# Kernel optimization log

Measured on AMD Instinct MI355X. Metric: run time of the kernel, lower is better.

Reference implementation:

```python
import jax, jax.numpy as jnp
import numpy as np

B, P, H, D, CLASSES, L = 2048, 1024, 2048, 256, 10, 10
EP = 1e-64
LOG2PI = float(np.log(2.0 * np.pi))


def setup_inputs() -> dict:
    key = jax.random.key(0)
    ks = jax.random.split(key, 16)
    s = 0.05
    return {
        "data": jax.random.normal(ks[0], (B, P), dtype=jnp.float32),
        "mask": jax.random.randint(ks[1], (B, P), 0, 2) > 0,
        "enc_w1": jax.random.normal(ks[2], (P, H), dtype=jnp.float32) * s,
        "enc_b1": jnp.zeros((H,), jnp.float32),
        "enc_w2": jax.random.normal(ks[3], (H, 2 * D), dtype=jnp.float32) * s,
        "enc_b2": jnp.zeros((2 * D,), jnp.float32),
        "dec_w1": jax.random.normal(ks[4], (D, H), dtype=jnp.float32) * s,
        "dec_b1": jnp.zeros((H,), jnp.float32),
        "dec_w2": jax.random.normal(ks[5], (H, 3 * P), dtype=jnp.float32) * s,
        "dec_b2": jnp.zeros((3 * P,), jnp.float32),
        "cls_w1": jax.random.normal(ks[6], (P, H), dtype=jnp.float32) * s,
        "cls_b1": jnp.zeros((H,), jnp.float32),
        "cls_w2": jax.random.normal(ks[7], (H, CLASSES), dtype=jnp.float32) * s,
        "cls_b2": jnp.zeros((CLASSES,), jnp.float32),
    }


def _student_t_logprob(x, loc, scale, df):
    y = (x - loc) / scale
    return (jax.lax.lgamma((df + 1.0) * 0.5) - jax.lax.lgamma(df * 0.5)
            - 0.5 * jnp.log(df * jnp.pi) - jnp.log(scale)
            - 0.5 * (df + 1.0) * jnp.log1p(y * y / df))


def reference(data, mask, enc_w1, enc_b1, enc_w2, enc_b2,
              dec_w1, dec_b1, dec_w2, dec_b2,
              cls_w1, cls_b1, cls_w2, cls_b2):
    maskf = mask.astype(data.dtype)
    key = jax.random.key(42)
    k_eps, k_t = jax.random.split(key)

    # encoder
    he = jax.nn.relu(data @ enc_w1 + enc_b1)
    out_enc = he @ enc_w2 + enc_b2                      # [B, 2D]
    mu, sig = out_enc[:, :D], jax.nn.softplus(out_enc[:, D:]) + EP

    # reparameterized q(z|x) samples, L draws
    eps = jax.random.normal(k_eps, (L, B, D), dtype=data.dtype)
    z = mu[None] + sig[None] * eps                      # [L, B, D]
    zf = z.reshape(L * B, D)

    # decoder -> StudentT params
    hd = jax.nn.relu(zf @ dec_w1 + dec_b1)
    out_dec = hd @ dec_w2 + dec_b2                      # [L*B, 3P]
    means = out_dec[:, :P]
    scales = jax.nn.softplus(out_dec[:, P:2 * P]) + 0.001
    dfree = jax.nn.softplus(out_dec[:, 2 * P:]) + 3.0

    data_t = jnp.tile(data, (L, 1))                     # [L*B, P]
    mask_t = jnp.tile(maskf, (L, 1))
    logpx = _student_t_logprob(data_t, means, scales, dfree)
    logpxobs = jnp.sum(logpx * mask_t, axis=1).reshape(L, B)

    logpz = jnp.sum(-0.5 * z * z, axis=-1) - 0.5 * D * LOG2PI          # [L, B]
    logq = jnp.sum(-0.5 * eps * eps - jnp.log(sig)[None], axis=-1) - 0.5 * D * LOG2PI

    imp_w = jax.nn.softmax(logpxobs + logpz - logq, axis=0)            # [L, B]

    # non-reparameterized StudentT sample (torch .sample() is detached)
    t = jax.random.t(k_t, dfree, shape=dfree.shape)
    xms = jax.lax.stop_gradient(means + scales * t).reshape(L, B, P)
    xm = jnp.einsum('ki,kij->ij', imp_w, xms)

    data_imputed = jnp.where(mask, data, xm)
    hc = jax.nn.relu(data_imputed @ cls_w1 + cls_b1)
    logits = hc @ cls_w2 + cls_b2
    return (data_imputed, logits)
```

## Files before the change

### kernel.cpp

```cpp
#include <hip/hip_runtime.h>
#include <math.h>

typedef unsigned int u32;
typedef unsigned short u16;
typedef __attribute__((ext_vector_type(8))) short bf16x8;
typedef __attribute__((ext_vector_type(16))) float f32x16;

struct U2 { u32 a, b; };

__host__ __device__ __forceinline__ U2 tf2x32(u32 k0, u32 k1, u32 c0, u32 c1) {
  u32 ks2 = k0 ^ k1 ^ 0x1BD11BDAu;
  u32 x0 = c0 + k0, x1 = c1 + k1;
#define TFR(r) { x0 += x1; x1 = (x1 << (r)) | (x1 >> (32 - (r))); x1 ^= x0; }
  TFR(13) TFR(15) TFR(26) TFR(6)
  x0 += k1; x1 += ks2 + 1u;
  TFR(17) TFR(29) TFR(16) TFR(24)
  x0 += ks2; x1 += k0 + 2u;
  TFR(13) TFR(15) TFR(26) TFR(6)
  x0 += k0; x1 += k1 + 3u;
  TFR(17) TFR(29) TFR(16) TFR(24)
  x0 += k1; x1 += ks2 + 4u;
  TFR(13) TFR(15) TFR(26) TFR(6)
  x0 += ks2; x1 += k0 + 5u;
#undef TFR
  return {x0, x1};
}

__host__ __device__ __forceinline__ u32 prf32(u32 k0, u32 k1, u32 i) {
  U2 r = tf2x32(k0, k1, 0u, i);
  return r.a ^ r.b;
}

__device__ __forceinline__ float u01_from_bits(u32 bits) {
  u32 r = (bits >> 9) | 0x3f800000u;
  return __uint_as_float(r) - 1.0f;
}

__device__ __forceinline__ float erfinv_f32(float x) {
  float w = -log1pf(-x * x);
  float p;
  if (w < 5.0f) {
    w -= 2.5f;
    p = 2.81022636e-08f;
    p = fmaf(p, w, 3.43273939e-07f);
    p = fmaf(p, w, -3.5233877e-06f);
    p = fmaf(p, w, -4.39150654e-06f);
    p = fmaf(p, w, 0.00021858087f);
    p = fmaf(p, w, -0.00125372503f);
    p = fmaf(p, w, -0.00417768164f);
    p = fmaf(p, w, 0.246640727f);
    p = fmaf(p, w, 1.50140941f);
  } else {
    w = sqrtf(w) - 3.0f;
    p = -0.000200214257f;
    p = fmaf(p, w, 0.000100950558f);
    p = fmaf(p, w, 0.00134934322f);
    p = fmaf(p, w, -0.00367342844f);
    p = fmaf(p, w, 0.00573950773f);
    p = fmaf(p, w, -0.0076224613f);
    p = fmaf(p, w, 0.00943887047f);
    p = fmaf(p, w, 1.00167406f);
    p = fmaf(p, w, 2.83297682f);
  }
  return p * x;
}

__device__ __forceinline__ float normal_from_bits(u32 bits) {
  const float lo = -0.99999994f;
  float u = u01_from_bits(bits) * 2.0f + lo;
  u = fmaxf(lo, u);
  return 1.41421356237f * erfinv_f32(u);
}

__device__ __forceinline__ float softplus_f(float x) {
  return fmaxf(x, 0.0f) + log1pf(expf(-fabsf(x)));
}

struct GI { bool acc; float V; u32 k0, k1; };
__device__ __forceinline__ GI gamma_iter(u32 k0, u32 k1, float d, float c) {
  U2 nk = tf2x32(k0, k1, 0u, 0u);
  U2 xk = tf2x32(k0, k1, 0u, 1u);
  U2 uk = tf2x32(k0, k1, 0u, 2u);
  u32 xk0 = xk.a, xk1 = xk.b;
  float x, v;
  do {
    U2 nxt = tf2x32(xk0, xk1, 0u, 0u);
    U2 sub = tf2x32(xk0, xk1, 0u, 1u);
    xk0 = nxt.a; xk1 = nxt.b;
    x = normal_from_bits(prf32(sub.a, sub.b, 0u));
    v = 1.0f + x * c;
  } while (v <= 0.0f);
  float X = x * x;
  float V = (v * v) * v;
  float U = u01_from_bits(prf32(uk.a, uk.b, 0u));
  bool cont = (U >= 1.0f - 0.0331f * (X * X)) &&
              (logf(U) >= 0.5f * X + d * ((1.0f - V) + logf(V)));
  GI r; r.acc = !cont; r.V = V; r.k0 = nk.a; r.k1 = nk.b;
  return r;
}

__device__ __forceinline__ float lgamma_half_diff(float x) {
  float z = x + 3.0f;
  float num = x * (x + 1.0f) * (x + 2.0f);
  float den = (x + 0.5f) * (x + 1.5f) * (x + 2.5f);
  float zh = z + 0.5f;
  float iz = 1.0f / z, izh = 1.0f / zh;
  float corr = 0.0833333333f * (izh - iz)
             - 0.00277777778f * (izh * izh * izh - iz * iz * iz);
  return logf(num / den) + 0.5f * logf(z) + z * log1pf(0.5f * iz) - 0.5f + corr;
}

__device__ __forceinline__ u16 f2bf(float f) {
  u32 u = __float_as_uint(f);
  u32 r = ((u >> 16) & 1u) + 0x7fffu;
  return (u16)((u + r) >> 16);
}
__device__ __forceinline__ float bf2f(u16 h) { return __uint_as_float(((u32)h) << 16); }

__device__ __forceinline__ void split2(float v, u16& h, u16& m) {
  h = f2bf(v);
  m = f2bf(v - bf2f(h));
}

#define GLOAD16(gp, lp) __builtin_amdgcn_global_load_lds( \
    (const __attribute__((address_space(1))) void*)(gp),  \
    (__attribute__((address_space(3))) void*)(lp), 16, 0, 0)

template<bool RELU, bool SIX>
__global__ __launch_bounds__(256, 3) void gemm_s3(const u16* __restrict__ A2,
                                                  const u16* __restrict__ B2T,
                                                  const float* __restrict__ bias,
                                                  float* __restrict__ Cf,
                                                  u16* __restrict__ C2,
                                                  int N, int kbits) {
  __shared__ u16 As[128 * 64];
  __shared__ u16 Bs[128 * 64];
  const int tid = threadIdx.x;
  const int l = tid & 63, w = tid >> 6;
  const int m0 = blockIdx.y * 128, n0 = blockIdx.x * 128;
  const int K2 = 2 << kbits;
  const int srow = l >> 3;
  const int scol = ((l & 7) ^ srow) << 3;
  const u16* agr[4]; const u16* bgr[4]; u16* al[4]; u16* bl[4];
#pragma unroll
  for (int j = 0; j < 4; ++j) {
    int r = w * 32 + j * 8 + srow;
    agr[j] = A2 + (size_t)(m0 + r) * K2 + scol;
    bgr[j] = B2T + (size_t)(n0 + r) * K2 + scol;
    al[j] = &As[(w * 4 + j) * 512];
    bl[j] = &Bs[(w * 4 + j) * 512];
  }
  f32x16 acc[2][2] = {};
  const int fr = l & 31;
  const int wm = w >> 1, wn = w & 1;
  const int swz = (l & 7) << 4;
  const int hk16 = (l >> 5) << 4;
  const int nk = 3 << (kbits - 6);
  const int kmask = (1 << kbits) - 1;
  for (int kt = 0; kt < nk; ++kt) {
    int vb = kt << 6;
    int s = vb >> kbits;
    int ko = vb & kmask;
    int ao = ((s >> 1) << kbits) + ko;
    int bo = ((s & 1) << kbits) + ko;
    __syncthreads();
#pragma unroll
    for (int j = 0; j < 4; ++j) {
      GLOAD16(agr[j] + ao, al[j]);
      GLOAD16(bgr[j] + bo, bl[j]);
    }
    __syncthreads();
#pragma unroll
    for (int ks = 0; ks < 4; ++ks) {
      bf16x8 af[2], bf[2];
#pragma unroll
      for (int mi = 0; mi < 2; ++mi) {
        int ar = wm * 64 + mi * 32 + fr;
        af[mi] = *(const bf16x8*)((const char*)As + ar * 128 + ((ks * 32 + hk16) ^ swz));
      }
#pragma unroll
      for (int ni = 0; ni < 2; ++ni) {
        int br = wn * 64 + ni * 32 + fr;
        bf[ni] = *(const bf16x8*)((const char*)Bs + br * 128 + ((ks * 32 + hk16) ^ swz));
      }
#pragma unroll
      for (int mi = 0; mi < 2; ++mi)
#pragma unroll
        for (int ni = 0; ni < 2; ++ni)
          acc[mi][ni] = __builtin_amdgcn_mfma_f32_32x32x16_bf16(af[mi], bf[ni], acc[mi][ni], 0, 0, 0);
    }
  }
#pragma unroll
  for (int mi = 0; mi < 2; ++mi)
#pragma unroll
  for (int ni = 0; ni < 2; ++ni) {
    int gcol = n0 + wn * 64 + ni * 32 + fr;
    float bsv = bias[gcol];
#pragma unroll
    for (int r = 0; r < 16; ++r) {
      int grow = m0 + wm * 64 + mi * 32 + (r & 3) + 8 * (r >> 2) + 4 * (l >> 5);
      float v = acc[mi][ni][r] + bsv;
      if (RELU) v = fmaxf(v, 0.0f);
      if (!SIX) {
        Cf[(size_t)grow * N + gcol] = v;
      } else {
        u16 h, mm; split2(v, h, mm);
        u16* q = C2 + (size_t)grow * 2 * N + gcol;
        q[0] = h; q[N] = mm;
      }
    }
  }
}

__global__ __launch_bounds__(256) void k_wconv(const float* __restrict__ W, u16* __restrict__ W2T,
                                               int K, int N) {
  __shared__ float t[64][65];
  const int k0 = blockIdx.y * 64, n0 = blockIdx.x * 64;
  const int tid = threadIdx.x;
  for (int i = tid; i < 4096; i += 256) {
    int kk = i >> 6, nn = i & 63;
    t[kk][nn] = W[(size_t)(k0 + kk) * N + (n0 + nn)];
  }
  __syncthreads();
  const int nn = tid >> 2, kc = (tid & 3) << 4;
  u16* base = W2T + (size_t)(n0 + nn) * 2 * K + (k0 + kc);
#pragma unroll
  for (int kk = 0; kk < 16; ++kk) {
    u16 h, m; split2(t[kc + kk][nn], h, m);
    base[kk] = h; base[K + kk] = m;
  }
}

__global__ __launch_bounds__(256) void k_aconv(const float* __restrict__ X, u16* __restrict__ X2,
                                               int total, int kbits) {
  int i = blockIdx.x * 256 + threadIdx.x;
  if (i >= total) return;
  int K = 1 << kbits;
  int r = i >> kbits, k = i & (K - 1);
  u16 h, m; split2(X[i], h, m);
  u16* q = X2 + ((size_t)r * 2 << kbits) + k;
  q[0] = h; q[K] = m;
}

__global__ __launch_bounds__(256) void k_build(const int* __restrict__ mask,
                                               u16* __restrict__ lists,
                                               int* __restrict__ nmiss) {
  const int b = blockIdx.x, tid = threadIdx.x;
  const int* mrow = mask + b * 1024;
  const int pb = tid * 4;
  int m0 = (mrow[pb] == 0), m1 = (mrow[pb + 1] == 0),
      m2 = (mrow[pb + 2] == 0), m3 = (mrow[pb + 3] == 0);
  int cnt = m0 + m1 + m2 + m3;
  __shared__ int sc[256];
  sc[tid] = cnt;
  __syncthreads();
  for (int off = 1; off < 256; off <<= 1) {
    int v = 0;
    if (tid >= off) v = sc[tid - off];
    __syncthreads();
    sc[tid] += v;
    __syncthreads();
  }
  int pos = sc[tid] - cnt;
  int nmT = sc[255];
  u16* lr = lists + b * 1024;
  int mpos = pos;
  int opos = nmT + (pb - pos);
  if (m0) lr[mpos++] = (u16)pb;       else lr[opos++] = (u16)pb;
  if (m1) lr[mpos++] = (u16)(pb + 1); else lr[opos++] = (u16)(pb + 1);
  if (m2) lr[mpos++] = (u16)(pb + 2); else lr[opos++] = (u16)(pb + 2);
  if (m3) lr[mpos++] = (u16)(pb + 3); else lr[opos++] = (u16)(pb + 3);
  if (tid == 255) nmiss[b] = nmT;
}

__global__ __launch_bounds__(256) void k_eps_z(const float* __restrict__ out_enc,
                                               u16* __restrict__ z2c,
                                               float* __restrict__ logpz,
                                               float* __restrict__ logq,
                                               int l0, u32 ke0, u32 ke1) {
  const int row = blockIdx.x;
  const int lb = l0 * 2048 + row;
  const int b = row & 2047;
  const int d = threadIdx.x;
  const u32 m = ((u32)lb << 8) + (u32)d;
  float mu = out_enc[b * 512 + d];
  float sg = softplus_f(out_enc[b * 512 + 256 + d]);
  float e = normal_from_bits(prf32(ke0, ke1, m));
  float zz = mu + sg * e;
  u16 h, mm; split2(zz, h, mm);
  u16* q = z2c + row * 512 + d;
  q[0] = h; q[256] = mm;
  float t1 = -0.5f * e * e - logf(sg);
  float t2 = -0.5f * zz * zz;
#pragma unroll
  for (int o = 32; o; o >>= 1) { t1 += __shfl_down(t1, o); t2 += __shfl_down(t2, o); }
  __shared__ float sm1[4], sm2[4];
  int lane = d & 63, wv = d >> 6;
  if (!lane) { sm1[wv] = t1; sm2[wv] = t2; }
  __syncthreads();
  if (d == 0) {
    float a = sm1[0] + sm1[1] + sm1[2] + sm1[3];
    float qq = sm2[0] + sm2[1] + sm2[2] + sm2[3];
    logq[lb]  = a - 235.2482645003962f;
    logpz[lb] = qq - 235.2482645003962f;
  }
}

__global__ __launch_bounds__(256) void k_lpx(const float* __restrict__ odec,
                                             const float* __restrict__ data,
                                             const u16* __restrict__ lists,
                                             const int* __restrict__ nmiss,
                                             float* __restrict__ lpxobs,
                                             int l0) {
  const int row = blockIdx.x;
  const int lb = l0 * 2048 + row;
  const int b = row & 2047;
  const int tid = threadIdx.x;
  const int nm = nmiss[b];
  const u16* orow = lists + b * 1024 + nm;
  const int no = 1024 - nm;
  float lpsum = 0.0f;
  for (int t = tid; t < no; t += 256) {
    int p = orow[t];
    float mean  = odec[(size_t)row * 3072 + p];
    float scale = softplus_f(odec[(size_t)row * 3072 + 1024 + p]) + 0.001f;
    float dfv   = softplus_f(odec[(size_t)row * 3072 + 2048 + p]) + 3.0f;
    float x = data[b * 1024 + p];
    float y = (x - mean) / scale;
    float lp = lgamma_half_diff(dfv * 0.5f)
             - 0.5f * logf(dfv * 3.14159274f) - logf(scale)
             - 0.5f * (dfv + 1.0f) * log1pf(y * y / dfv);
    lpsum += lp;
  }
#pragma unroll
  for (int o = 32; o; o >>= 1) lpsum += __shfl_down(lpsum, o);
  __shared__ float sm[4];
  int lane = tid & 63, wv = tid >> 6;
  if (!lane) sm[wv] = lpsum;
  __syncthreads();
  if (tid == 0) lpxobs[lb] = sm[0] + sm[1] + sm[2] + sm[3];
}

__global__ __launch_bounds__(256) void k_sample(const float* __restrict__ odec,
                                                const u16* __restrict__ lists,
                                                const int* __restrict__ nmiss,
                                                u16* __restrict__ xms,
                                                int l0, u32 kn0, u32 kn1, u32 kg0, u32 kg1) {
  const int row = blockIdx.x;
  const int lb = l0 * 2048 + row;
  const int b = row & 2047;
  const int nm = nmiss[b];
  const u16* mr = lists + b * 1024;
  __shared__ u32 qk0[1024], qk1[1024];
  __shared__ u16 qp[1024];
  __shared__ int qn;
  if (threadIdx.x == 0) qn = 0;
  __syncthreads();
  for (int t = threadIdx.x; t < nm; t += 256) {
    int p = mr[t];
    float mean  = odec[(size_t)row * 3072 + p];
    float scale = softplus_f(odec[(size_t)row * 3072 + 1024 + p]) + 0.001f;
    float dfv   = softplus_f(odec[(size_t)row * 3072 + 2048 + p]) + 3.0f;
    u32 i = ((u32)lb << 10) + (u32)p;
    float n = normal_from_bits(prf32(kn0, kn1, i));
    U2 gk = tf2x32(kg0, kg1, 0u, i);
    U2 kk = tf2x32(gk.a, gk.b, 0u, 0u);
    float half_df = dfv * 0.5f;
    float d = half_df - 0.33333334f;
    float c = 0.33333334f / sqrtf(d);
    GI r = gamma_iter(kk.a, kk.b, d, c);
    if (r.acc) {
      float g = d * r.V;
      xms[i] = f2bf(mean + scale * (n * sqrtf(half_df / g)));
    } else {
      int s = atomicAdd(&qn, 1);
      qk0[s] = r.k0; qk1[s] = r.k1; qp[s] = (u16)p;
    }
  }
  __syncthreads();
  int n2 = qn;
  for (int t = threadIdx.x; t < n2; t += 256) {
    int p = qp[t];
    float mean  = odec[(size_t)row * 3072 + p];
    float scale = softplus_f(odec[(size_t)row * 3072 + 1024 + p]) + 0.001f;
    float dfv   = softplus_f(odec[(size_t)row * 3072 + 2048 + p]) + 3.0f;
    u32 i = ((u32)lb << 10) + (u32)p;
    float n = normal_from_bits(prf32(kn0, kn1, i));
    float half_df = dfv * 0.5f;
    float d = half_df - 0.33333334f;
    float c = 0.33333334f / sqrtf(d);
    u32 k0 = qk0[t], k1 = qk1[t];
    GI r;
    do { r = gamma_iter(k0, k1, d, c); k0 = r.k0; k1 = r.k1; } while (!r.acc);
    float g = d * r.V;
    xms[i] = f2bf(mean + scale * (n * sqrtf(half_df / g)));
  }
}

__global__ __launch_bounds__(256) void k_impw(const float* __restrict__ lpx,
                                              const float* __restrict__ lpz,
                                              const float* __restrict__ lq,
                                              float* __restrict__ w) {
  int b = blockIdx.x * 256 + threadIdx.x;
  float s[10], mx = -INFINITY;
#pragma unroll
  for (int l = 0; l < 10; ++l) {
    s[l] = lpx[l * 2048 + b] + lpz[l * 2048 + b] - lq[l * 2048 + b];
    mx = fmaxf(mx, s[l]);
  }
  float se = 0.0f;
#pragma unroll
  for (int l = 0; l < 10; ++l) { s[l] = expf(s[l] - mx); se += s[l]; }
#pragma unroll
  for (int l = 0; l < 10; ++l) w[l * 2048 + b] = s[l] / se;
}

__global__ __launch_bounds__(256) void k_xm(const int* __restrict__ mask,
                                            const float* __restrict__ data,
                                            const float* __restrict__ impw,
                                            const u16* __restrict__ xms,
                                            u16* __restrict__ imp2,
                                            float* __restrict__ out) {
  int idx = blockIdx.x * 256 + threadIdx.x;
  int b = idx >> 10, p = idx & 1023;
  float o;
  if (mask[idx]) {
    o = data[idx];
  } else {
    float acc = 0.0f;
#pragma unroll
    for (int l = 0; l < 10; ++l)
      acc += impw[l * 2048 + b] * bf2f(xms[((size_t)l * 2048 + b) * 1024 + p]);
    o = acc;
  }
  out[idx] = o;
  u16 h, m; split2(o, h, m);
  u16* q = imp2 + (size_t)b * 2048 + p;
  q[0] = h; q[1024] = m;
}

__global__ __launch_bounds__(256) void k_cls2(const float* __restrict__ hc,
                                              const float* __restrict__ w2,
                                              const float* __restrict__ b2,
                                              float* __restrict__ out) {
  int b = blockIdx.x, tid = threadIdx.x;
  float acc[10];
#pragma unroll
  for (int c = 0; c < 10; ++c) acc[c] = 0.0f;
  for (int k = tid; k < 2048; k += 256) {
    float h = hc[(size_t)b * 2048 + k];
#pragma unroll
    for (int c = 0; c < 10; ++c) acc[c] = fmaf(h, w2[k * 10 + c], acc[c]);
  }
  __shared__ float red[4][10];
  int lane = tid & 63, wv = tid >> 6;
#pragma unroll
  for (int c = 0; c < 10; ++c) {
    float v = acc[c];
#pragma unroll
    for (int o = 32; o; o >>= 1) v += __shfl_down(v, o);
    if (!lane) red[wv][c] = v;
  }
  __syncthreads();
  if (tid < 10) out[b * 10 + tid] = red[0][tid] + red[1][tid] + red[2][tid] + red[3][tid] + b2[tid];
}

extern "C" void kernel_launch(void* const* d_in, const int* in_sizes, int n_in,
                              void* d_out, int out_size, void* d_ws, size_t ws_size,
                              hipStream_t stream) {
  const float* data   = (const float*)d_in[0];
  const int*   mask   = (const int*)d_in[1];
  const float* enc_w1 = (const float*)d_in[2];
  const float* enc_b1 = (const float*)d_in[3];
  const float* enc_w2 = (const float*)d_in[4];
  const float* enc_b2 = (const float*)d_in[5];
  const float* dec_w1 = (const float*)d_in[6];
  const float* dec_b1 = (const float*)d_in[7];
  const float* dec_w2 = (const float*)d_in[8];
  const float* dec_b2 = (const float*)d_in[9];
  const float* cls_w1 = (const float*)d_in[10];
  const float* cls_b1 = (const float*)d_in[11];
  const float* cls_w2 = (const float*)d_in[12];
  const float* cls_b2 = (const float*)d_in[13];

  float* out = (float*)d_out;
  char* wsb = (char*)d_ws;

  if (ws_size < 186982400ULL) return;

  u16*   xmsu   = (u16*)(wsb + 0);
  u16*   w_d2   = (u16*)(wsb + 41943040);
  u16*   w_d1   = (u16*)(wsb + 67108864);
  u16*   hx2    = (u16*)(wsb + 69206016);
  float* odec   = (float*)(wsb + 102760448);
  u16*   z2c    = (u16*)(wsb + 153092096);
  u16*   data2  = (u16*)(wsb + 157286400);
  u16*   w_ec   = (u16*)(wsb + 165675008);
  u16*   w_e2   = (u16*)(wsb + 174063616);
  float* logpz  = (float*)(wsb + 178257920);
  float* logq   = (float*)(wsb + 178339840);
  float* lpxobs = (float*)(wsb + 178421760);
  float* impw   = (float*)(wsb + 178503680);
  float* out_enc= (float*)(wsb + 178585600);
  u16*   lists  = (u16*)(wsb + 182779904);
  int*   nmiss  = (int*)(wsb + 186974208);
  float* hc     = odec;
  u16*   imp2   = data2;

  U2 ke = tf2x32(0u, 42u, 0u, 0u);
  U2 kt = tf2x32(0u, 42u, 0u, 1u);
  U2 kn = tf2x32(kt.a, kt.b, 0u, 0u);
  U2 kg = tf2x32(kt.a, kt.b, 0u, 1u);

  dim3 blk(256);
  k_aconv<<<8192, blk, 0, stream>>>(data, data2, 2097152, 10);
  k_wconv<<<dim3(32, 16), blk, 0, stream>>>(enc_w1, w_ec, 1024, 2048);
  k_wconv<<<dim3(8, 32),  blk, 0, stream>>>(enc_w2, w_e2, 2048, 512);
  k_wconv<<<dim3(48, 32), blk, 0, stream>>>(dec_w2, w_d2, 2048, 3072);
  k_wconv<<<dim3(32, 4),  blk, 0, stream>>>(dec_w1, w_d1, 256, 2048);
  k_build<<<2048, blk, 0, stream>>>(mask, lists, nmiss);

  gemm_s3<true,  true ><<<dim3(16, 16), blk, 0, stream>>>(data2, w_ec, enc_b1, nullptr, hx2, 2048, 10);
  gemm_s3<false, false><<<dim3(4, 16),  blk, 0, stream>>>(hx2, w_e2, enc_b2, out_enc, nullptr, 512, 11);

  for (int l0 = 0; l0 < 10; l0 += 2) {
    k_eps_z<<<4096, blk, 0, stream>>>(out_enc, z2c, logpz, logq, l0, ke.a, ke.b);
    gemm_s3<true,  true ><<<dim3(16, 32), blk, 0, stream>>>(z2c, w_d1, dec_b1, nullptr, hx2, 2048, 8);
    gemm_s3<false, false><<<dim3(24, 32), blk, 0, stream>>>(hx2, w_d2, dec_b2, odec, nullptr, 3072, 11);
    k_lpx<<<4096, blk, 0, stream>>>(odec, data, lists, nmiss, lpxobs, l0);
    k_sample<<<4096, blk, 0, stream>>>(odec, lists, nmiss, xmsu, l0, kn.a, kn.b, kg.a, kg.b);
  }

  k_impw<<<8, blk, 0, stream>>>(lpxobs, logpz, logq, impw);
  k_xm<<<8192, blk, 0, stream>>>(mask, data, impw, xmsu, imp2, out);

  k_wconv<<<dim3(32, 16), blk, 0, stream>>>(cls_w1, w_ec, 1024, 2048);
  gemm_s3<true, false><<<dim3(16, 16), blk, 0, stream>>>(imp2, w_ec, cls_b1, hc, nullptr, 2048, 10);
  k_cls2<<<2048, blk, 0, stream>>>(hc, cls_w2, cls_b2, out + 2048 * 1024);
}
```

Baseline: 1.845 ms.

## Fuse lpx and sampling kernels, hoist eps/z generation, swizzle decoder GEMM grid

Merges the per-chunk log-likelihood and Student-T sampling kernels into one post-processing kernel, so each odec row is read while still likely in cache and one launch is saved per chunk. The eps/z generation now runs once for all L draws ahead of the loop, writing into a larger workspace buffer. The large decoder output GEMM gets an XCD-aware block-index swizzle for better L2 locality, and the GEMM launch bounds move from 3 to 4 blocks per CU. The cost is extra workspace and a longer combined kernel whose LDS use may limit occupancy.

```diff
diff --git a/kernel.cpp b/kernel.cpp
--- a/kernel.cpp
+++ b/kernel.cpp
@@ -126,8 +126,8 @@
     (const __attribute__((address_space(1))) void*)(gp),  \
     (__attribute__((address_space(3))) void*)(lp), 16, 0, 0)
 
-template<bool RELU, bool SIX>
-__global__ __launch_bounds__(256, 3) void gemm_s3(const u16* __restrict__ A2,
+template<bool RELU, bool SIX, bool SWZ>
+__global__ __launch_bounds__(256, 4) void gemm_s3(const u16* __restrict__ A2,
                                                   const u16* __restrict__ B2T,
                                                   const float* __restrict__ bias,
                                                   float* __restrict__ Cf,
@@ -137,7 +137,15 @@
   __shared__ u16 Bs[128 * 64];
   const int tid = threadIdx.x;
   const int l = tid & 63, w = tid >> 6;
-  const int m0 = blockIdx.y * 128, n0 = blockIdx.x * 128;
+  int bx = blockIdx.x, by = blockIdx.y;
+  if (SWZ) {
+    int nx = gridDim.x;
+    int wg = by * nx + bx;
+    int per = (nx * gridDim.y) >> 3;
+    int sw = (wg & 7) * per + (wg >> 3);
+    bx = sw % nx; by = sw / nx;
+  }
+  const int m0 = by * 128, n0 = bx * 128;
   const int K2 = 2 << kbits;
   const int srow = l >> 3;
   const int scol = ((l & 7) ^ srow) << 3;
@@ -274,13 +282,12 @@
 }
 
 __global__ __launch_bounds__(256) void k_eps_z(const float* __restrict__ out_enc,
-                                               u16* __restrict__ z2c,
+                                               u16* __restrict__ z2all,
                                                float* __restrict__ logpz,
                                                float* __restrict__ logq,
-                                               int l0, u32 ke0, u32 ke1) {
-  const int row = blockIdx.x;
-  const int lb = l0 * 2048 + row;
-  const int b = row & 2047;
+                                               u32 ke0, u32 ke1) {
+  const int lb = blockIdx.x;
+  const int b = lb & 2047;
   const int d = threadIdx.x;
   const u32 m = ((u32)lb << 8) + (u32)d;
   float mu = out_enc[b * 512 + d];
@@ -288,7 +295,7 @@
   float e = normal_from_bits(prf32(ke0, ke1, m));
   float zz = mu + sg * e;
   u16 h, mm; split2(zz, h, mm);
-  u16* q = z2c + row * 512 + d;
+  u16* q = z2all + (size_t)lb * 512 + d;
   q[0] = h; q[256] = mm;
   float t1 = -0.5f * e * e - logf(sg);
   float t2 = -0.5f * zz * zz;
@@ -306,17 +313,23 @@
   }
 }
 
-__global__ __launch_bounds__(256) void k_lpx(const float* __restrict__ odec,
-                                             const float* __restrict__ data,
-                                             const u16* __restrict__ lists,
-                                             const int* __restrict__ nmiss,
-                                             float* __restrict__ lpxobs,
-                                             int l0) {
+__global__ __launch_bounds__(256) void k_post(const float* __restrict__ odec,
+                                              const float* __restrict__ data,
+                                              const u16* __restrict__ lists,
+                                              const int* __restrict__ nmiss,
+                                              float* __restrict__ lpxobs,
+                                              u16* __restrict__ xms,
+                                              int l0, u32 kn0, u32 kn1, u32 kg0, u32 kg1) {
   const int row = blockIdx.x;
   const int lb = l0 * 2048 + row;
   const int b = row & 2047;
   const int tid = threadIdx.x;
   const int nm = nmiss[b];
+  __shared__ u32 qk0[1024], qk1[1024];
+  __shared__ u16 qp[1024];
+  __shared__ int qn;
+  __shared__ float sm[4];
+  if (tid == 0) qn = 0;
   const u16* orow = lists + b * 1024 + nm;
   const int no = 1024 - nm;
   float lpsum = 0.0f;
@@ -327,36 +340,18 @@
     float dfv   = softplus_f(odec[(size_t)row * 3072 + 2048 + p]) + 3.0f;
     float x = data[b * 1024 + p];
     float y = (x - mean) / scale;
-    float lp = lgamma_half_diff(dfv * 0.5f)
-             - 0.5f * logf(dfv * 3.14159274f) - logf(scale)
-             - 0.5f * (dfv + 1.0f) * log1pf(y * y / dfv);
-    lpsum += lp;
+    lpsum += lgamma_half_diff(dfv * 0.5f)
+           - 0.5f * logf(dfv * 3.14159274f) - logf(scale)
+           - 0.5f * (dfv + 1.0f) * log1pf(y * y / dfv);
   }
 #pragma unroll
   for (int o = 32; o; o >>= 1) lpsum += __shfl_down(lpsum, o);
-  __shared__ float sm[4];
   int lane = tid & 63, wv = tid >> 6;
   if (!lane) sm[wv] = lpsum;
   __syncthreads();
   if (tid == 0) lpxobs[lb] = sm[0] + sm[1] + sm[2] + sm[3];
-}
-
-__global__ __launch_bounds__(256) void k_sample(const float* __restrict__ odec,
-                                                const u16* __restrict__ lists,
-                                                const int* __restrict__ nmiss,
-                                                u16* __restrict__ xms,
-                                                int l0, u32 kn0, u32 kn1, u32 kg0, u32 kg1) {
-  const int row = blockIdx.x;
-  const int lb = l0 * 2048 + row;
-  const int b = row & 2047;
-  const int nm = nmiss[b];
   const u16* mr = lists + b * 1024;
-  __shared__ u32 qk0[1024], qk1[1024];
-  __shared__ u16 qp[1024];
-  __shared__ int qn;
-  if (threadIdx.x == 0) qn = 0;
-  __syncthreads();
-  for (int t = threadIdx.x; t < nm; t += 256) {
+  for (int t = tid; t < nm; t += 256) {
     int p = mr[t];
     float mean  = odec[(size_t)row * 3072 + p];
     float scale = softplus_f(odec[(size_t)row * 3072 + 1024 + p]) + 0.001f;
@@ -379,7 +374,7 @@
   }
   __syncthreads();
   int n2 = qn;
-  for (int t = threadIdx.x; t < n2; t += 256) {
+  for (int t = tid; t < n2; t += 256) {
     int p = qp[t];
     float mean  = odec[(size_t)row * 3072 + p];
     float scale = softplus_f(odec[(size_t)row * 3072 + 1024 + p]) + 0.001f;
@@ -486,14 +481,13 @@
   float* out = (float*)d_out;
   char* wsb = (char*)d_ws;
 
-  if (ws_size < 186982400ULL) return;
+  if (ws_size < 207953920ULL) return;
 
   u16*   xmsu   = (u16*)(wsb + 0);
   u16*   w_d2   = (u16*)(wsb + 41943040);
   u16*   w_d1   = (u16*)(wsb + 67108864);
   u16*   hx2    = (u16*)(wsb + 69206016);
   float* odec   = (float*)(wsb + 102760448);
-  u16*   z2c    = (u16*)(wsb + 153092096);
   u16*   data2  = (u16*)(wsb + 157286400);
   u16*   w_ec   = (u16*)(wsb + 165675008);
   u16*   w_e2   = (u16*)(wsb + 174063616);
@@ -504,6 +498,7 @@
   float* out_enc= (float*)(wsb + 178585600);
   u16*   lists  = (u16*)(wsb + 182779904);
   int*   nmiss  = (int*)(wsb + 186974208);
+  u16*   z2all  = (u16*)(wsb + 186982400);
   float* hc     = odec;
   u16*   imp2   = data2;
 
@@ -520,21 +515,21 @@
   k_wconv<<<dim3(32, 4),  blk, 0, stream>>>(dec_w1, w_d1, 256, 2048);
   k_build<<<2048, blk, 0, stream>>>(mask, lists, nmiss);
 
-  gemm_s3<true,  true ><<<dim3(16, 16), blk, 0, stream>>>(data2, w_ec, enc_b1, nullptr, hx2, 2048, 10);
-  gemm_s3<false, false><<<dim3(4, 16),  blk, 0, stream>>>(hx2, w_e2, enc_b2, out_enc, nullptr, 512, 11);
+  gemm_s3<true,  true,  false><<<dim3(16, 16), blk, 0, stream>>>(data2, w_ec, enc_b1, nullptr, hx2, 2048, 10);
+  gemm_s3<false, false, false><<<dim3(4, 16),  blk, 0, stream>>>(hx2, w_e2, enc_b2, out_enc, nullptr, 512, 11);
+
+  k_eps_z<<<20480, blk, 0, stream>>>(out_enc, z2all, logpz, logq, ke.a, ke.b);
 
   for (int l0 = 0; l0 < 10; l0 += 2) {
-    k_eps_z<<<4096, blk, 0, stream>>>(out_enc, z2c, logpz, logq, l0, ke.a, ke.b);
-    gemm_s3<true,  true ><<<dim3(16, 32), blk, 0, stream>>>(z2c, w_d1, dec_b1, nullptr, hx2, 2048, 8);
-    gemm_s3<false, false><<<dim3(24, 32), blk, 0, stream>>>(hx2, w_d2, dec_b2, odec, nullptr, 3072, 11);
-    k_lpx<<<4096, blk, 0, stream>>>(odec, data, lists, nmiss, lpxobs, l0);
-    k_sample<<<4096, blk, 0, stream>>>(odec, lists, nmiss, xmsu, l0, kn.a, kn.b, kg.a, kg.b);
+    gemm_s3<true,  true,  false><<<dim3(16, 32), blk, 0, stream>>>(z2all + (size_t)l0 * 2048 * 512, w_d1, dec_b1, nullptr, hx2, 2048, 8);
+    gemm_s3<false, false, true ><<<dim3(24, 32), blk, 0, stream>>>(hx2, w_d2, dec_b2, odec, nullptr, 3072, 11);
+    k_post<<<4096, blk, 0, stream>>>(odec, data, lists, nmiss, lpxobs, xmsu, l0, kn.a, kn.b, kg.a, kg.b);
   }
 
   k_impw<<<8, blk, 0, stream>>>(lpxobs, logpz, logq, impw);
   k_xm<<<8192, blk, 0, stream>>>(mask, data, impw, xmsu, imp2, out);
 
   k_wconv<<<dim3(32, 16), blk, 0, stream>>>(cls_w1, w_ec, 1024, 2048);
-  gemm_s3<true, false><<<dim3(16, 16), blk, 0, stream>>>(imp2, w_ec, cls_b1, hc, nullptr, 2048, 10);
+  gemm_s3<true, false, false><<<dim3(16, 16), blk, 0, stream>>>(imp2, w_ec, cls_b1, hc, nullptr, 2048, 10);
   k_cls2<<<2048, blk, 0, stream>>>(hc, cls_w2, cls_b2, out + 2048 * 1024);
 }
```

Measured after the change: 1.843 ms. No clear change (-0.1%).
